# Optimization experiments

Measured on AMD Instinct MI355X. Metric: run time of the kernel, lower is better.

Reference implementation:

```python
import jax, jax.numpy as jnp
import numpy as np

N, E = 50000, 800000
IN, HID, HEADS, OUT = 128, 64, 4, 256
HC = HID * HEADS  # 256
NEG_SLOPE = 0.2
LN_EPS = 1e-5


def setup_inputs() -> dict:
    key = jax.random.key(0)
    ks = jax.random.split(key, 20)
    s = 0.02
    inp = {
        "x": jax.random.normal(ks[0], (N, IN), jnp.float32),
        "edge_index": jax.random.randint(ks[1], (2, E), 0, N, jnp.int64),
        "w_in": jax.random.normal(ks[2], (IN, HID), jnp.float32) * s,
        "b_in": jnp.zeros((HID,), jnp.float32),
        "lin0_w": jax.random.normal(ks[3], (HID, HC), jnp.float32) * s,
        "att_src0": jax.random.normal(ks[4], (HEADS, HID), jnp.float32) * s,
        "att_dst0": jax.random.normal(ks[5], (HEADS, HID), jnp.float32) * s,
        "bias0": jnp.zeros((HC,), jnp.float32),
        "ln0_g": jnp.ones((HC,), jnp.float32),
        "ln0_b": jnp.zeros((HC,), jnp.float32),
        "lin1_w": jax.random.normal(ks[6], (HC, HC), jnp.float32) * s,
        "att_src1": jax.random.normal(ks[7], (HEADS, HID), jnp.float32) * s,
        "att_dst1": jax.random.normal(ks[8], (HEADS, HID), jnp.float32) * s,
        "bias1": jnp.zeros((HC,), jnp.float32),
        "ln1_g": jnp.ones((HC,), jnp.float32),
        "ln1_b": jnp.zeros((HC,), jnp.float32),
        "w_out": jax.random.normal(ks[9], (HC, OUT), jnp.float32) * s,
        "b_out": jnp.zeros((OUT,), jnp.float32),
    }
    return inp


def _gat_conv(x, src, dst, lin_w, att_s, att_d, bias):
    # x: [N, F_in]; src/dst: [E'] (self loops included); output [N, HEADS*HID]
    n = x.shape[0]
    h = (x @ lin_w).reshape(n, HEADS, HID)                     # [N,H,C]
    a_s = jnp.einsum('nhc,hc->nh', h, att_s)                   # [N,H]
    a_d = jnp.einsum('nhc,hc->nh', h, att_d)
    e = jax.nn.leaky_relu(a_s[src] + a_d[dst], NEG_SLOPE)      # [E',H]
    # scatter-softmax over edges grouped by destination node
    m = jax.ops.segment_max(e, dst, num_segments=n)            # [N,H]
    ex = jnp.exp(e - m[dst])
    z = jax.ops.segment_sum(ex, dst, num_segments=n)
    alpha = ex / (z[dst] + 1e-16)                              # [E',H]
    msg = h[src] * alpha[:, :, None]                           # [E',H,C]
    out = jax.ops.segment_sum(msg, dst, num_segments=n)        # [N,H,C]
    return out.reshape(n, HEADS * HID) + bias


def _layernorm(x, g, b):
    mu = x.mean(-1, keepdims=True)
    var = ((x - mu) ** 2).mean(-1, keepdims=True)
    return (x - mu) * jax.lax.rsqrt(var + LN_EPS) * g + b


def reference(x, edge_index, w_in, b_in,
              lin0_w, att_src0, att_dst0, bias0, ln0_g, ln0_b,
              lin1_w, att_src1, att_dst1, bias1, ln1_g, ln1_b,
              w_out, b_out):
    n = x.shape[0]
    # PyG GATConv adds self loops by default
    loop = jnp.arange(n, dtype=edge_index.dtype)
    src = jnp.concatenate([edge_index[0], loop])
    dst = jnp.concatenate([edge_index[1], loop])

    h = jax.nn.relu(x @ w_in + b_in)                           # input_proj + relu
    h = _gat_conv(h, src, dst, lin0_w, att_src0, att_dst0, bias0)
    h = jax.nn.relu(_layernorm(h, ln0_g, ln0_b))               # dropout: eval mode (identity)
    h = _gat_conv(h, src, dst, lin1_w, att_src1, att_dst1, bias1)
    h = jax.nn.relu(_layernorm(h, ln1_g, ln1_b))
    g = h.mean(axis=0)                                         # mean pool over nodes
    return g @ w_out + b_out                                   # [OUT]
```

## Files before the change

kernel.cpp:

```cpp
#include <hip/hip_runtime.h>

#define NN 50000
#define EE 800000
#define EP (EE + NN)
#define NH 4
#define HC 256
#define NOUT 256
#define NEG_SLOPE 0.2f
#define LN_EPS 1e-5f
#define CHUNK 64
#define NPART 64
#define SLOTS 64

typedef unsigned short u16;
typedef __attribute__((ext_vector_type(8))) short bf16x8;
typedef __attribute__((ext_vector_type(8))) unsigned short ushort8;
typedef __attribute__((ext_vector_type(4))) float f32x4;
typedef __attribute__((ext_vector_type(2))) float f32x2;

__device__ __forceinline__ u16 f2bf(float f) {
    unsigned int u = __float_as_uint(f);
    u += 0x7fff + ((u >> 16) & 1);
    return (u16)(u >> 16);
}
__device__ __forceinline__ float bf2f(u16 s) {
    return __uint_as_float(((unsigned int)s) << 16);
}
__device__ __forceinline__ int permL(int s) {
    return (s >> 6) * 64 + (s & 3) * 16 + ((s & 63) >> 2);
}

__global__ void k_prep(const float* __restrict__ w_in, const float* __restrict__ lin0_w,
                       const float* __restrict__ lin1_w,
                       const float* __restrict__ atts0, const float* __restrict__ attd0,
                       const float* __restrict__ bias1, const float* __restrict__ ln1g,
                       const float* __restrict__ ln1b,
                       u16* __restrict__ winT, u16* __restrict__ w0T, u16* __restrict__ w1T,
                       float* __restrict__ avs, float* __restrict__ avd,
                       float* __restrict__ biasP, float* __restrict__ gP, float* __restrict__ bP,
                       int* __restrict__ cursor, float* __restrict__ gaccP,
                       const int* __restrict__ raw, int* __restrict__ flag) {
    int b = blockIdx.x, t = threadIdx.x;
    if (b < 352) {
        int i = b * 256 + t;
        if (i < 8192)       { int k = i >> 6,  j = i & 63;  winT[j * 128 + k] = f2bf(w_in[i]); }
        else if (i < 24576) {
            int i2 = i - 8192;  int k = i2 >> 8, j = i2 & 255;
            int s = ((k & 15) << 2) | (k >> 4);
            w0T[j * 64 + s] = f2bf(lin0_w[i2]);
        }
        else if (i < 90112) { int i2 = i - 24576; int k = i2 >> 8, j = i2 & 255; w1T[j * 256 + k] = f2bf(lin1_w[i2]); }
    } else if (b < 548) {
        int i = (b - 352) * 256 + t;
        if (i < NN) cursor[i] = 0;
    } else if (b < 612) {
        gaccP[(b - 548) * 256 + t] = 0.f;
    } else if (b == 612) {
        __shared__ int any;
        if (t == 0) any = 0;
        __syncthreads();
        int found = 0;
        for (int i = t; i < 4096; i += 256)
            if (raw[2 * i + 1] != 0) found = 1;
        if (found) atomicOr(&any, 1);
        __syncthreads();
        if (t == 0) *flag = any;
    } else if (b == 613) {
        int k = t >> 2, h = t & 3;
        float ss = 0.f, dd = 0.f;
        for (int c = 0; c < 64; ++c) {
            float w = lin0_w[k * HC + h * 64 + c];
            ss += w * atts0[h * 64 + c];
            dd += w * attd0[h * 64 + c];
        }
        avs[t] = ss; avd[t] = dd;
    } else {
        int L = permL(t);
        biasP[t] = bias1[L];
        gP[t]    = ln1g[L];
        bP[t]    = ln1b[L];
    }
}

__global__ void k_scatter(const int* __restrict__ raw, const int* __restrict__ flag,
                          int* __restrict__ cursor, int* __restrict__ esrc2) {
    const int T = (EP + 3) / 4;
    int tid = blockIdx.x * 256 + threadIdx.x;
    if (tid >= T) return;
    int f = *flag;
    #pragma unroll
    for (int i = 0; i < 4; ++i) {
        int e = tid + i * T;
        if (e >= EP) continue;
        if (e >= EE) {
            int d = e - EE;
            esrc2[d * SLOTS] = d;
        } else {
            int s, d;
            if (f) { s = raw[e];     d = raw[EE + e]; }
            else   { s = raw[2 * e]; d = raw[2 * (EE + e)]; }
            int r = atomicAdd(&cursor[d], 1);
            if (r < SLOTS - 1) esrc2[d * SLOTS + 1 + r] = s;
        }
    }
}

__global__ void k_proj_mfma(const float* __restrict__ x, const u16* __restrict__ wT,
                            const float* __restrict__ bias,
                            const float* __restrict__ avs, const float* __restrict__ avd,
                            unsigned int* __restrict__ h08,
                            float* __restrict__ as_, float* __restrict__ ad_) {
    __shared__ float4 s_avs[64], s_avd[64];
    int wave = threadIdx.x >> 6, lane = threadIdx.x & 63;
    int lr = lane & 15, lk = lane >> 4;
    if (threadIdx.x < 64) {
        s_avs[threadIdx.x] = *(const float4*)&avs[threadIdx.x * 4];
        s_avd[threadIdx.x] = *(const float4*)&avd[threadIdx.x * 4];
    }
    __syncthreads();
    int rowbase = (blockIdx.x * 4 + wave) * 64;
    f32x4 acc[4][4];
    #pragma unroll
    for (int mf = 0; mf < 4; ++mf)
        #pragma unroll
        for (int nf = 0; nf < 4; ++nf) acc[mf][nf] = (f32x4)0.f;
    for (int kk = 0; kk < 128; kk += 32) {
        bf16x8 a[4], b[4];
        #pragma unroll
        for (int mf = 0; mf < 4; ++mf) {
            int row = rowbase + mf * 16 + lr;
            if (row < NN) {
                float4 v0 = *(const float4*)&x[(size_t)row * 128 + kk + lk * 8];
                float4 v1 = *(const float4*)&x[(size_t)row * 128 + kk + lk * 8 + 4];
                a[mf][0] = (short)f2bf(v0.x); a[mf][1] = (short)f2bf(v0.y);
                a[mf][2] = (short)f2bf(v0.z); a[mf][3] = (short)f2bf(v0.w);
                a[mf][4] = (short)f2bf(v1.x); a[mf][5] = (short)f2bf(v1.y);
                a[mf][6] = (short)f2bf(v1.z); a[mf][7] = (short)f2bf(v1.w);
            } else a[mf] = (bf16x8)(short)0;
        }
        #pragma unroll
        for (int nf = 0; nf < 4; ++nf)
            b[nf] = *(const bf16x8*)&wT[(size_t)(nf * 16 + lr) * 128 + kk + lk * 8];
        #pragma unroll
        for (int mf = 0; mf < 4; ++mf)
            #pragma unroll
            for (int nf = 0; nf < 4; ++nf)
                acc[mf][nf] = __builtin_amdgcn_mfma_f32_16x16x32_bf16(a[mf], b[nf], acc[mf][nf], 0, 0, 0);
    }
    #pragma unroll
    for (int mf = 0; mf < 4; ++mf)
        #pragma unroll
        for (int r = 0; r < 4; ++r) {
            int row = rowbase + mf * 16 + lk * 4 + r;
            float4 ps = make_float4(0.f, 0.f, 0.f, 0.f);
            float4 pd = make_float4(0.f, 0.f, 0.f, 0.f);
            float vv[4];
            #pragma unroll
            for (int nf = 0; nf < 4; ++nf) {
                int col = nf * 16 + lr;
                float v = fmaxf(acc[mf][nf][r] + bias[col], 0.f);
                vv[nf] = v;
                float4 vs = s_avs[col], vd = s_avd[col];
                ps.x += v * vs.x; ps.y += v * vs.y; ps.z += v * vs.z; ps.w += v * vs.w;
                pd.x += v * vd.x; pd.y += v * vd.y; pd.z += v * vd.z; pd.w += v * vd.w;
            }
            unsigned int pk = (unsigned int)__builtin_amdgcn_cvt_pk_fp8_f32(vv[0], vv[1], 0, false);
            pk = (unsigned int)__builtin_amdgcn_cvt_pk_fp8_f32(vv[2], vv[3], (int)pk, true);
            if (row < NN) h08[(size_t)row * 16 + lr] = pk;
            #pragma unroll
            for (int o = 1; o < 16; o <<= 1) {
                ps.x += __shfl_xor(ps.x, o, 64); ps.y += __shfl_xor(ps.y, o, 64);
                ps.z += __shfl_xor(ps.z, o, 64); ps.w += __shfl_xor(ps.w, o, 64);
                pd.x += __shfl_xor(pd.x, o, 64); pd.y += __shfl_xor(pd.y, o, 64);
                pd.z += __shfl_xor(pd.z, o, 64); pd.w += __shfl_xor(pd.w, o, 64);
            }
            if (lr == 0 && row < NN) {
                *(float4*)&as_[row * NH] = ps;
                *(float4*)&ad_[row * NH] = pd;
            }
        }
}

__global__ void k_agg64(const int* __restrict__ cursor, const int* __restrict__ esrc2,
                        const unsigned int* __restrict__ h08, const float* __restrict__ as_,
                        const float* __restrict__ ad_, u16* __restrict__ agg) {
    __shared__ float sw[4][CHUNK][4];
    __shared__ int   ss[4][CHUNK];
    int wave = threadIdx.x >> 6, lane = threadIdx.x & 63;
    int n = blockIdx.x * 4 + wave;
    int cnt = cursor[n]; cnt = cnt > SLOTS - 1 ? SLOTS - 1 : cnt;
    int start = n * SLOTS, end = start + cnt + 1;
    float4 adv = *(const float4*)&ad_[n * NH];
    int p = lane & 15, grp = lane >> 4;
    f32x2 acc2[4][2];
    #pragma unroll
    for (int h = 0; h < 4; ++h) { acc2[h][0] = (f32x2)0.f; acc2[h][1] = (f32x2)0.f; }
    float z0 = 0.f, z1 = 0.f, z2 = 0.f, z3 = 0.f;

    for (int base = start; base < end; base += CHUNK) {
        int m = end - base; if (m > CHUNK) m = CHUNK;
        {
            int s = 0; float4 w4 = make_float4(0.f, 0.f, 0.f, 0.f);
            if (lane < m) {
                s = esrc2[base + lane];
                float4 asv = *(const float4*)&as_[s * NH];
                float e0 = asv.x + adv.x; e0 = e0 > 0.f ? e0 : e0 * NEG_SLOPE; w4.x = __expf(e0);
                float e1 = asv.y + adv.y; e1 = e1 > 0.f ? e1 : e1 * NEG_SLOPE; w4.y = __expf(e1);
                float e2 = asv.z + adv.z; e2 = e2 > 0.f ? e2 : e2 * NEG_SLOPE; w4.z = __expf(e2);
                float e3 = asv.w + adv.w; e3 = e3 > 0.f ? e3 : e3 * NEG_SLOPE; w4.w = __expf(e3);
            }
            ss[wave][lane] = s;
            *(float4*)&sw[wave][lane][0] = w4;
            z0 += w4.x; z1 += w4.y; z2 += w4.z; z3 += w4.w;
        }
        int e = grp;
        int s = ss[wave][e];
        float4 w4 = *(const float4*)&sw[wave][e][0];
        unsigned int q = h08[s * 16 + p];
        int nIter = (m + 3) >> 2;
        for (int it = 0; it < nIter; ++it) {
            int en = (e + 4) & (CHUNK - 1);
            int sn = ss[wave][en];
            float4 w4n = *(const float4*)&sw[wave][en][0];
            unsigned int qn = h08[sn * 16 + p];
            f32x2 p01 = __builtin_amdgcn_cvt_pk_f32_fp8((int)q, false);
            f32x2 p23 = __builtin_amdgcn_cvt_pk_f32_fp8((int)q, true);
            acc2[0][0] += (f32x2)w4.x * p01; acc2[0][1] += (f32x2)w4.x * p23;
            acc2[1][0] += (f32x2)w4.y * p01; acc2[1][1] += (f32x2)w4.y * p23;
            acc2[2][0] += (f32x2)w4.z * p01; acc2[2][1] += (f32x2)w4.z * p23;
            acc2[3][0] += (f32x2)w4.w * p01; acc2[3][1] += (f32x2)w4.w * p23;
            e = en; w4 = w4n; q = qn;
        }
    }
    #pragma unroll
    for (int h = 0; h < 4; ++h)
        #pragma unroll
        for (int j = 0; j < 2; ++j) {
            acc2[h][j][0] += __shfl_xor(acc2[h][j][0], 16, 64);
            acc2[h][j][0] += __shfl_xor(acc2[h][j][0], 32, 64);
            acc2[h][j][1] += __shfl_xor(acc2[h][j][1], 16, 64);
            acc2[h][j][1] += __shfl_xor(acc2[h][j][1], 32, 64);
        }
    #pragma unroll
    for (int o = 32; o >= 1; o >>= 1) {
        z0 += __shfl_xor(z0, o, 64);
        z1 += __shfl_xor(z1, o, 64);
        z2 += __shfl_xor(z2, o, 64);
        z3 += __shfl_xor(z3, o, 64);
    }
    if (grp == 0) {
        float iz[4] = {1.f / (z0 + 1e-16f), 1.f / (z1 + 1e-16f),
                       1.f / (z2 + 1e-16f), 1.f / (z3 + 1e-16f)};
        #pragma unroll
        for (int h = 0; h < 4; ++h) {
            ushort4 yv;
            yv.x = f2bf(acc2[h][0][0] * iz[h]);
            yv.y = f2bf(acc2[h][0][1] * iz[h]);
            yv.z = f2bf(acc2[h][1][0] * iz[h]);
            yv.w = f2bf(acc2[h][1][1] * iz[h]);
            *(ushort4*)&agg[(size_t)n * HC + h * 64 + p * 4] = yv;
        }
    }
}

__global__ __launch_bounds__(256) void k_mid(
        const u16* __restrict__ agg, const u16* __restrict__ w0T,
        const float* __restrict__ bias0, const float* __restrict__ g0, const float* __restrict__ b0,
        const u16* __restrict__ w1T,
        const float* __restrict__ atts1, const float* __restrict__ attd1,
        unsigned int* __restrict__ hp8,
        float* __restrict__ as_, float* __restrict__ ad_) {
    __shared__ __align__(16) u16 h1sh[64 * 256];
    __shared__ float stat[64][4][2];
    __shared__ float murs[64][2];
    int wave = threadIdx.x >> 6, lane = threadIdx.x & 63;
    int lr = lane & 15, lk = lane >> 4;
    int rowbase = blockIdx.x * 64;

    f32x4 acc[4][4];
    #pragma unroll
    for (int mf = 0; mf < 4; ++mf)
        #pragma unroll
        for (int nf = 0; nf < 4; ++nf) acc[mf][nf] = (f32x4)0.f;
    for (int kk = 0; kk < 64; kk += 32) {
        bf16x8 a[4], bv[4];
        #pragma unroll
        for (int mf = 0; mf < 4; ++mf) {
            int row = rowbase + mf * 16 + lr;
            a[mf] = (row < NN) ? *(const bf16x8*)&agg[(size_t)row * HC + wave * 64 + kk + lk * 8]
                               : (bf16x8)(short)0;
        }
        #pragma unroll
        for (int nf = 0; nf < 4; ++nf)
            bv[nf] = *(const bf16x8*)&w0T[(size_t)(wave * 64 + nf * 16 + lr) * 64 + kk + lk * 8];
        #pragma unroll
        for (int mf = 0; mf < 4; ++mf)
            #pragma unroll
            for (int nf = 0; nf < 4; ++nf)
                acc[mf][nf] = __builtin_amdgcn_mfma_f32_16x16x32_bf16(a[mf], bv[nf], acc[mf][nf], 0, 0, 0);
    }
    float bcol[4];
    #pragma unroll
    for (int nf = 0; nf < 4; ++nf) bcol[nf] = bias0[wave * 64 + nf * 16 + lr];
    #pragma unroll
    for (int mf = 0; mf < 4; ++mf)
        #pragma unroll
        for (int r = 0; r < 4; ++r) {
            float s = 0.f, q = 0.f;
            #pragma unroll
            for (int nf = 0; nf < 4; ++nf) {
                float xv = acc[mf][nf][r] + bcol[nf];
                s += xv; q += xv * xv;
            }
            #pragma unroll
            for (int o = 1; o < 16; o <<= 1) {
                s += __shfl_xor(s, o, 64);
                q += __shfl_xor(q, o, 64);
            }
            if (lr == 0) {
                int row = mf * 16 + lk * 4 + r;
                stat[row][wave][0] = s;
                stat[row][wave][1] = q;
            }
        }
    __syncthreads();
    if (threadIdx.x < 64) {
        int row = threadIdx.x;
        float S = stat[row][0][0] + stat[row][1][0] + stat[row][2][0] + stat[row][3][0];
        float Q = stat[row][0][1] + stat[row][1][1] + stat[row][2][1] + stat[row][3][1];
        float mu = S * (1.f / HC);
        float var = Q * (1.f / HC) - mu * mu;
        murs[row][0] = mu;
        murs[row][1] = rsqrtf(var + LN_EPS);
    }
    __syncthreads();
    #pragma unroll
    for (int mf = 0; mf < 4; ++mf)
        #pragma unroll
        for (int r = 0; r < 4; ++r) {
            int lrow = mf * 16 + lk * 4 + r;
            float mu = murs[lrow][0], rs = murs[lrow][1];
            #pragma unroll
            for (int nf = 0; nf < 4; ++nf) {
                int col = wave * 64 + nf * 16 + lr;
                float xv = acc[mf][nf][r] + bcol[nf];
                u16 y = f2bf(fmaxf((xv - mu) * rs * g0[col] + b0[col], 0.f));
                int byte = (lrow * 512 + col * 2) ^ ((lrow & 7) << 4);
                *(u16*)((char*)h1sh + byte) = y;
            }
        }
    __syncthreads();

    f32x4 acc2[4][4];
    #pragma unroll
    for (int mf = 0; mf < 4; ++mf)
        #pragma unroll
        for (int nf = 0; nf < 4; ++nf) acc2[mf][nf] = (f32x4)0.f;
    for (int kk = 0; kk < 256; kk += 32) {
        bf16x8 a[4], bv[4];
        #pragma unroll
        for (int mf = 0; mf < 4; ++mf) {
            int row = mf * 16 + lr;
            int byte = (row * 512 + (kk + lk * 8) * 2) ^ ((row & 7) << 4);
            a[mf] = *(const bf16x8*)((const char*)h1sh + byte);
        }
        #pragma unroll
        for (int nf = 0; nf < 4; ++nf)
            bv[nf] = *(const bf16x8*)&w1T[(size_t)(wave * 64 + nf * 16 + lr) * 256 + kk + lk * 8];
        #pragma unroll
        for (int mf = 0; mf < 4; ++mf)
            #pragma unroll
            for (int nf = 0; nf < 4; ++nf)
                acc2[mf][nf] = __builtin_amdgcn_mfma_f32_16x16x32_bf16(a[mf], bv[nf], acc2[mf][nf], 0, 0, 0);
    }
    float asv[4], adv[4];
    #pragma unroll
    for (int nf = 0; nf < 4; ++nf) {
        int col = wave * 64 + nf * 16 + lr;
        asv[nf] = atts1[col];
        adv[nf] = attd1[col];
    }
    #pragma unroll
    for (int mf = 0; mf < 4; ++mf)
        #pragma unroll
        for (int r = 0; r < 4; ++r) {
            int row = rowbase + mf * 16 + lk * 4 + r;
            float v0 = acc2[mf][0][r], v1 = acc2[mf][1][r];
            float v2 = acc2[mf][2][r], v3 = acc2[mf][3][r];
            float ps = v0 * asv[0] + v1 * asv[1] + v2 * asv[2] + v3 * asv[3];
            float pd = v0 * adv[0] + v1 * adv[1] + v2 * adv[2] + v3 * adv[3];
            unsigned int pk = (unsigned int)__builtin_amdgcn_cvt_pk_fp8_f32(v0, v1, 0, false);
            pk = (unsigned int)__builtin_amdgcn_cvt_pk_fp8_f32(v2, v3, (int)pk, true);
            if (row < NN) hp8[(size_t)row * 64 + wave * 16 + lr] = pk;
            #pragma unroll
            for (int o = 1; o < 16; o <<= 1) {
                ps += __shfl_xor(ps, o, 64);
                pd += __shfl_xor(pd, o, 64);
            }
            if (lr == 0 && row < NN) {
                as_[row * NH + wave] = ps;
                ad_[row * NH + wave] = pd;
            }
        }
}

__global__ void k_agg_ln8(const int* __restrict__ cursor, const int* __restrict__ esrc2,
                          const unsigned int* __restrict__ hp8, const float* __restrict__ as_,
                          const float* __restrict__ ad_,
                          const float* __restrict__ biasP, const float* __restrict__ gP,
                          const float* __restrict__ bP, float* __restrict__ gaccP) {
    __shared__ float sw[4][CHUNK][4];
    __shared__ int   ss[4][CHUNK];
    __shared__ float pool[4][16][17];
    int wave = threadIdx.x >> 6, lane = threadIdx.x & 63;
    int n = blockIdx.x * 4 + wave;
    int cnt = cursor[n]; cnt = cnt > SLOTS - 1 ? SLOTS - 1 : cnt;
    int start = n * SLOTS, end = start + cnt + 1;
    float4 adv = *(const float4*)&ad_[n * NH];
    int p = lane & 15, grp = lane >> 4;
    int c = p * 16, hd = p >> 2;
    f32x2 acc2[8];
    #pragma unroll
    for (int j = 0; j < 8; ++j) acc2[j] = (f32x2)0.f;
    float z0 = 0.f, z1 = 0.f, z2 = 0.f, z3 = 0.f;

    for (int base = start; base < end; base += CHUNK) {
        int m = end - base; if (m > CHUNK) m = CHUNK;
        if (lane < m) {
            int s = esrc2[base + lane];
            float4 asv = *(const float4*)&as_[s * NH];
            float e0 = asv.x + adv.x; e0 = e0 > 0.f ? e0 : e0 * NEG_SLOPE; float w0 = __expf(e0);
            float e1 = asv.y + adv.y; e1 = e1 > 0.f ? e1 : e1 * NEG_SLOPE; float w1 = __expf(e1);
            float e2 = asv.z + adv.z; e2 = e2 > 0.f ? e2 : e2 * NEG_SLOPE; float w2 = __expf(e2);
            float e3 = asv.w + adv.w; e3 = e3 > 0.f ? e3 : e3 * NEG_SLOPE; float w3 = __expf(e3);
            ss[wave][lane] = s;
            *(float4*)&sw[wave][lane][0] = make_float4(w0, w1, w2, w3);
            z0 += w0; z1 += w1; z2 += w2; z3 += w3;
        }
        int e = grp;
        bool vA = e < m;
        int sA = vA ? ss[wave][e] : 0;
        float wA = vA ? sw[wave][e][hd] : 0.f;
        uint4 qA = *(const uint4*)&hp8[(size_t)sA * 64 + p * 4];
        int eB = e + 4;
        bool vB = eB < m;
        int sB = vB ? ss[wave][eB] : 0;
        float wB = vB ? sw[wave][eB][hd] : 0.f;
        uint4 qB = *(const uint4*)&hp8[(size_t)sB * 64 + p * 4];
        int nIter = (m + 3) >> 2;
        for (int it = 0; it < nIter; ++it) {
            int en = e + 8;
            bool vn = en < m;
            int sn = vn ? ss[wave][en] : 0;
            float wn = vn ? sw[wave][en][hd] : 0.f;
            uint4 qn = *(const uint4*)&hp8[(size_t)sn * 64 + p * 4];
            f32x2 wv = (f32x2)wA;
            acc2[0] += wv * __builtin_amdgcn_cvt_pk_f32_fp8((int)qA.x, false);
            acc2[1] += wv * __builtin_amdgcn_cvt_pk_f32_fp8((int)qA.x, true);
            acc2[2] += wv * __builtin_amdgcn_cvt_pk_f32_fp8((int)qA.y, false);
            acc2[3] += wv * __builtin_amdgcn_cvt_pk_f32_fp8((int)qA.y, true);
            acc2[4] += wv * __builtin_amdgcn_cvt_pk_f32_fp8((int)qA.z, false);
            acc2[5] += wv * __builtin_amdgcn_cvt_pk_f32_fp8((int)qA.z, true);
            acc2[6] += wv * __builtin_amdgcn_cvt_pk_f32_fp8((int)qA.w, false);
            acc2[7] += wv * __builtin_amdgcn_cvt_pk_f32_fp8((int)qA.w, true);
            e += 4;
            qA = qB; wA = wB;
            qB = qn; wB = wn;
        }
    }
    #pragma unroll
    for (int j = 0; j < 8; ++j) {
        acc2[j][0] += __shfl_xor(acc2[j][0], 16, 64);
        acc2[j][0] += __shfl_xor(acc2[j][0], 32, 64);
        acc2[j][1] += __shfl_xor(acc2[j][1], 16, 64);
        acc2[j][1] += __shfl_xor(acc2[j][1], 32, 64);
    }
    #pragma unroll
    for (int o = 32; o >= 1; o >>= 1) {
        z0 += __shfl_xor(z0, o, 64);
        z1 += __shfl_xor(z1, o, 64);
        z2 += __shfl_xor(z2, o, 64);
        z3 += __shfl_xor(z3, o, 64);
    }
    float zh = hd == 0 ? z0 : hd == 1 ? z1 : hd == 2 ? z2 : z3;
    float iz = 1.f / (zh + 1e-16f);
    float xv[16], sum = 0.f;
    #pragma unroll
    for (int k = 0; k < 16; ++k) { xv[k] = acc2[k >> 1][k & 1] * iz + biasP[c + k]; sum += xv[k]; }
    #pragma unroll
    for (int o = 8; o >= 1; o >>= 1) sum += __shfl_xor(sum, o, 64);
    float mu = sum * (1.f / HC);
    float vs = 0.f;
    #pragma unroll
    for (int k = 0; k < 16; ++k) { float d = xv[k] - mu; vs += d * d; }
    #pragma unroll
    for (int o = 8; o >= 1; o >>= 1) vs += __shfl_xor(vs, o, 64);
    float rs = rsqrtf(vs * (1.f / HC) + LN_EPS);
    if (grp == 0) {
        #pragma unroll
        for (int k = 0; k < 16; ++k)
            pool[wave][p][k] = fmaxf((xv[k] - mu) * rs * gP[c + k] + bP[c + k], 0.f);
    }
    __syncthreads();
    int t = threadIdx.x;
    float s = pool[0][t >> 4][t & 15] + pool[1][t >> 4][t & 15]
            + pool[2][t >> 4][t & 15] + pool[3][t >> 4][t & 15];
    atomicAdd(&gaccP[(blockIdx.x & (NPART - 1)) * 256 + t], s);
}

__global__ void k_final(const float* __restrict__ gaccP, const float* __restrict__ w,
                        const float* __restrict__ b, float* __restrict__ out) {
    __shared__ float gs[256];
    int t = threadIdx.x;
    float s = 0.f;
    for (int pp = 0; pp < NPART; ++pp) s += gaccP[pp * 256 + t];
    gs[t] = s;
    __syncthreads();
    float acc = b[t];
    for (int k = 0; k < HC; ++k)
        acc += (gs[k] * (1.f / NN)) * w[permL(k) * NOUT + t];
    out[t] = acc;
}

extern "C" void kernel_launch(void* const* d_in, const int* in_sizes, int n_in,
                              void* d_out, int out_size, void* d_ws, size_t ws_size,
                              hipStream_t stream) {
    const float* x      = (const float*)d_in[0];
    const int*   eiraw  = (const int*)d_in[1];
    const float* w_in   = (const float*)d_in[2];
    const float* b_in   = (const float*)d_in[3];
    const float* lin0_w = (const float*)d_in[4];
    const float* atts0  = (const float*)d_in[5];
    const float* attd0  = (const float*)d_in[6];
    const float* bias0  = (const float*)d_in[7];
    const float* ln0g   = (const float*)d_in[8];
    const float* ln0b   = (const float*)d_in[9];
    const float* lin1_w = (const float*)d_in[10];
    const float* atts1  = (const float*)d_in[11];
    const float* attd1  = (const float*)d_in[12];
    const float* bias1  = (const float*)d_in[13];
    const float* ln1g   = (const float*)d_in[14];
    const float* ln1b   = (const float*)d_in[15];
    const float* w_out  = (const float*)d_in[16];
    const float* b_out  = (const float*)d_in[17];
    float* out = (float*)d_out;

    char* ws = (char*)d_ws;
    size_t off = 0;
    auto alloc = [&](size_t bytes) {
        void* p = ws + off;
        off = (off + bytes + 255) & ~(size_t)255;
        return p;
    };
    int*   esrc2  = (int*)  alloc((size_t)NN * SLOTS * 4 + 256);
    int*   cursor = (int*)  alloc((size_t)NN * 4);
    int*   flag   = (int*)  alloc(256);
    u16*   winT   = (u16*)  alloc((size_t)64 * 128 * 2);
    u16*   w0T    = (u16*)  alloc((size_t)256 * 64 * 2);
    u16*   w1T    = (u16*)  alloc((size_t)256 * 256 * 2);
    float* avs    = (float*)alloc(64 * 4 * 4);
    float* avd    = (float*)alloc(64 * 4 * 4);
    float* biasP  = (float*)alloc(HC * 4);
    float* gP     = (float*)alloc(HC * 4);
    float* bP     = (float*)alloc(HC * 4);
    unsigned int* h08 = (unsigned int*)alloc((size_t)NN * 16 * 4);
    u16*   hpb    = (u16*)  alloc((size_t)NN * HC * 2);
    unsigned int* hp8 = (unsigned int*)alloc((size_t)NN * 64 * 4);
    float* as_    = (float*)alloc((size_t)NN * NH * 4);
    float* ad_    = (float*)alloc((size_t)NN * NH * 4);
    float* as1_   = (float*)alloc((size_t)NN * NH * 4);
    float* ad1_   = (float*)alloc((size_t)NN * NH * 4);
    float* gaccP  = (float*)alloc((size_t)NPART * HC * 4);

    k_prep<<<615, 256, 0, stream>>>(w_in, lin0_w, lin1_w, atts0, attd0, bias1, ln1g, ln1b,
                                    winT, w0T, w1T, avs, avd, biasP, gP, bP,
                                    cursor, gaccP, eiraw, flag);
    k_scatter<<<((EP + 3) / 4 + 255) / 256, 256, 0, stream>>>(eiraw, flag, cursor, esrc2);

    k_proj_mfma<<<(NN + 255) / 256, 256, 0, stream>>>(x, winT, b_in, avs, avd, h08, as_, ad_);

    k_agg64<<<NN / 4, 256, 0, stream>>>(cursor, esrc2, h08, as_, ad_, hpb);

    k_mid<<<(NN + 63) / 64, 256, 0, stream>>>(hpb, w0T, bias0, ln0g, ln0b,
                                              w1T, atts1, attd1, hp8, as1_, ad1_);

    k_agg_ln8<<<NN / 4, 256, 0, stream>>>(cursor, esrc2, hp8, as1_, ad1_, biasP, gP, bP, gaccP);

    k_final<<<1, 256, 0, stream>>>(gaccP, w_out, b_out, out);
}
```

Measured before the change: 251.5 us.

## Merge edge scatter and input projection into one launch; single-pass LayerNorm stats

Fuses the edge-bucketing scatter kernel and the MFMA input projection into one grid, with blocks partitioned by index, so the two independent stages run concurrently and one launch is saved. The scatter now uses one edge per thread instead of four. Separately, the final LayerNorm computes sum and sum of squares in one pass, which removes a second reduction loop and its shuffles. The one-pass variance is less numerically robust than the two-pass form.

```diff
diff --git a/kernel.cpp b/kernel.cpp
--- a/kernel.cpp
+++ b/kernel.cpp
@@ -11,6 +11,8 @@
 #define CHUNK 64
 #define NPART 64
 #define SLOTS 64
+#define SCATB ((EP + 255) / 256)
+#define PROJB ((NN + 255) / 256)
 
 typedef unsigned short u16;
 typedef __attribute__((ext_vector_type(8))) short bf16x8;
@@ -82,35 +84,32 @@
     }
 }
 
-__global__ void k_scatter(const int* __restrict__ raw, const int* __restrict__ flag,
-                          int* __restrict__ cursor, int* __restrict__ esrc2) {
-    const int T = (EP + 3) / 4;
-    int tid = blockIdx.x * 256 + threadIdx.x;
-    if (tid >= T) return;
-    int f = *flag;
-    #pragma unroll
-    for (int i = 0; i < 4; ++i) {
-        int e = tid + i * T;
-        if (e >= EP) continue;
+__global__ __launch_bounds__(256) void k_scatprj(
+        const int* __restrict__ raw, const int* __restrict__ flag,
+        int* __restrict__ cursor, int* __restrict__ esrc2,
+        const float* __restrict__ x, const u16* __restrict__ wT,
+        const float* __restrict__ bias,
+        const float* __restrict__ avs, const float* __restrict__ avd,
+        unsigned int* __restrict__ h08,
+        float* __restrict__ as_, float* __restrict__ ad_) {
+    if (blockIdx.x < SCATB) {
+        int e = blockIdx.x * 256 + threadIdx.x;
+        if (e >= EP) return;
         if (e >= EE) {
             int d = e - EE;
             esrc2[d * SLOTS] = d;
         } else {
+            int f = *flag;
             int s, d;
             if (f) { s = raw[e];     d = raw[EE + e]; }
             else   { s = raw[2 * e]; d = raw[2 * (EE + e)]; }
             int r = atomicAdd(&cursor[d], 1);
             if (r < SLOTS - 1) esrc2[d * SLOTS + 1 + r] = s;
         }
-    }
-}
-
-__global__ void k_proj_mfma(const float* __restrict__ x, const u16* __restrict__ wT,
-                            const float* __restrict__ bias,
-                            const float* __restrict__ avs, const float* __restrict__ avd,
-                            unsigned int* __restrict__ h08,
-                            float* __restrict__ as_, float* __restrict__ ad_) {
+        return;
+    }
     __shared__ float4 s_avs[64], s_avd[64];
+    int pb = blockIdx.x - SCATB;
     int wave = threadIdx.x >> 6, lane = threadIdx.x & 63;
     int lr = lane & 15, lk = lane >> 4;
     if (threadIdx.x < 64) {
@@ -118,7 +117,7 @@
         s_avd[threadIdx.x] = *(const float4*)&avd[threadIdx.x * 4];
     }
     __syncthreads();
-    int rowbase = (blockIdx.x * 4 + wave) * 64;
+    int rowbase = (pb * 4 + wave) * 64;
     f32x4 acc[4][4];
     #pragma unroll
     for (int mf = 0; mf < 4; ++mf)
@@ -484,18 +483,19 @@
     }
     float zh = hd == 0 ? z0 : hd == 1 ? z1 : hd == 2 ? z2 : z3;
     float iz = 1.f / (zh + 1e-16f);
-    float xv[16], sum = 0.f;
-    #pragma unroll
-    for (int k = 0; k < 16; ++k) { xv[k] = acc2[k >> 1][k & 1] * iz + biasP[c + k]; sum += xv[k]; }
-    #pragma unroll
-    for (int o = 8; o >= 1; o >>= 1) sum += __shfl_xor(sum, o, 64);
+    float xv[16], sum = 0.f, sq = 0.f;
+    #pragma unroll
+    for (int k = 0; k < 16; ++k) {
+        xv[k] = acc2[k >> 1][k & 1] * iz + biasP[c + k];
+        sum += xv[k]; sq += xv[k] * xv[k];
+    }
+    #pragma unroll
+    for (int o = 8; o >= 1; o >>= 1) {
+        sum += __shfl_xor(sum, o, 64);
+        sq  += __shfl_xor(sq, o, 64);
+    }
     float mu = sum * (1.f / HC);
-    float vs = 0.f;
-    #pragma unroll
-    for (int k = 0; k < 16; ++k) { float d = xv[k] - mu; vs += d * d; }
-    #pragma unroll
-    for (int o = 8; o >= 1; o >>= 1) vs += __shfl_xor(vs, o, 64);
-    float rs = rsqrtf(vs * (1.f / HC) + LN_EPS);
+    float rs = rsqrtf(sq * (1.f / HC) - mu * mu + LN_EPS);
     if (grp == 0) {
         #pragma unroll
         for (int k = 0; k < 16; ++k)
@@ -575,9 +575,9 @@
     k_prep<<<615, 256, 0, stream>>>(w_in, lin0_w, lin1_w, atts0, attd0, bias1, ln1g, ln1b,
                                     winT, w0T, w1T, avs, avd, biasP, gP, bP,
                                     cursor, gaccP, eiraw, flag);
-    k_scatter<<<((EP + 3) / 4 + 255) / 256, 256, 0, stream>>>(eiraw, flag, cursor, esrc2);
-
-    k_proj_mfma<<<(NN + 255) / 256, 256, 0, stream>>>(x, winT, b_in, avs, avd, h08, as_, ad_);
+
+    k_scatprj<<<SCATB + PROJB, 256, 0, stream>>>(eiraw, flag, cursor, esrc2,
+                                                 x, winT, b_in, avs, avd, h08, as_, ad_);
 
     k_agg64<<<NN / 4, 256, 0, stream>>>(cursor, esrc2, h08, as_, ad_, hpb);
 
```

New measurement: 252.0 us. Within noise of the previous version (+0.2%).
